# Optimization experiments

Hardware: AMD Instinct MI355X
Metric: run time of the kernel (lower is better)

The kernel has to match this reference:

```python
import jax, jax.numpy as jnp
import numpy as np

N_NODES = 100000
N_EDGES = 1600000
IN_FT = 128
OUT_FT = 128


def setup_inputs() -> dict:
    key = jax.random.key(0)
    k1, k2, k3, k4, k5, k6 = jax.random.split(key, 6)
    stdv = 1.0 / np.sqrt(OUT_FT)
    x = jax.random.normal(k1, (N_NODES, IN_FT), dtype=jnp.float32)
    edge_rows = jax.random.randint(k2, (N_EDGES,), 0, N_NODES, dtype=jnp.int32)
    edge_cols = jax.random.randint(k3, (N_EDGES,), 0, N_NODES, dtype=jnp.int32)
    # normalized adjacency values (positive, like D^-1 A)
    edge_vals = jax.random.uniform(k4, (N_EDGES,), dtype=jnp.float32)
    W = jax.random.uniform(k5, (IN_FT, OUT_FT), dtype=jnp.float32, minval=-stdv, maxval=stdv)
    b = jax.random.uniform(k6, (OUT_FT,), dtype=jnp.float32, minval=-stdv, maxval=stdv)
    return {"x": x, "edge_rows": edge_rows, "edge_cols": edge_cols,
            "edge_vals": edge_vals, "W": W, "b": b}


def reference(x, edge_rows, edge_cols, edge_vals, W, b):
    # dense projection + bias: [N, out_ft]
    h = x @ W + b
    # SpMM: out[r] = sum_e vals[e] * h[cols[e]] for edges with rows[e] == r
    msgs = edge_vals[:, None] * h[edge_cols]          # [E, out_ft]
    out = jax.ops.segment_sum(msgs, edge_rows, num_segments=N_NODES)
    return jax.nn.relu(out)
```

## Files before the change

### kernel.cpp

```cpp
#include <hip/hip_runtime.h>

#define N_NODES 100000
#define N_EDGES 1600000
#define FT 128

#define NBUCK 391
#define EPB 4096
#define NBLKP ((N_EDGES + EPB - 1) / EPB)
#define CAP 1536

#define OFF_H 0
#define OFF_BUCKETED 25600000
#define OFF_BLKHIST 38400000
#define OFF_BTOT 39011524
#define OFF_BBASE 39013088
#define WS_NEEDED 39014656

typedef __attribute__((ext_vector_type(8))) short bf16x8;
typedef __attribute__((ext_vector_type(4))) float f32x4;

static __device__ __forceinline__ ushort f2bf(float f) {
  const unsigned u = __float_as_uint(f);
  return (ushort)((u + 0x7FFF + ((u >> 16) & 1)) >> 16);
}
static __device__ __forceinline__ float bf2f(ushort s) {
  return __uint_as_float((unsigned)s << 16);
}

__global__ __launch_bounds__(256) void gemm_bias_kernel(
    const float* __restrict__ x,
    const float* __restrict__ W,
    const float* __restrict__ b,
    ushort* __restrict__ h) {
  __shared__ __align__(16) ushort whi[16384];
  __shared__ __align__(16) ushort wlo[16384];

  const int tid = threadIdx.x;

  for (int idx = tid; idx < 16384; idx += 256) {
    const int k = idx >> 7;
    const int col = idx & 127;
    const float wv = W[idx];
    const ushort hi = f2bf(wv);
    const ushort lo = f2bf(wv - bf2f(hi));
    const int lane_ = (((k >> 3) & 3) << 4) | (col & 15);
    const int pos = ((((k >> 5) << 3) + (col >> 4)) * 64 + lane_) * 8 + (k & 7);
    whi[pos] = hi;
    wlo[pos] = lo;
  }
  __syncthreads();

  const int w = tid >> 6;
  const int lane = tid & 63;
  const int r0 = blockIdx.x * 256 + w * 64;
  const int arow = lane & 15;
  const int kgrp = (lane >> 4) << 3;

  float bias_v[8];
#pragma unroll
  for (int ct = 0; ct < 8; ++ct) bias_v[ct] = b[ct * 16 + (lane & 15)];

  f32x4 acc[4][8];
#pragma unroll
  for (int rf = 0; rf < 4; ++rf)
#pragma unroll
    for (int ct = 0; ct < 8; ++ct) acc[rf][ct] = (f32x4){0.f, 0.f, 0.f, 0.f};

#pragma unroll
  for (int ks = 0; ks < 4; ++ks) {
    bf16x8 afr[4];
#pragma unroll
    for (int rf = 0; rf < 4; ++rf) {
      int r = r0 + rf * 16 + arow;
      r = (r < N_NODES) ? r : (N_NODES - 1);
      const float* xp = x + (size_t)r * FT + ks * 32 + kgrp;
      const float4 u0 = *(const float4*)xp;
      const float4 u1 = *(const float4*)(xp + 4);
      bf16x8 a;
      a[0] = (short)f2bf(u0.x);
      a[1] = (short)f2bf(u0.y);
      a[2] = (short)f2bf(u0.z);
      a[3] = (short)f2bf(u0.w);
      a[4] = (short)f2bf(u1.x);
      a[5] = (short)f2bf(u1.y);
      a[6] = (short)f2bf(u1.z);
      a[7] = (short)f2bf(u1.w);
      afr[rf] = a;
    }
#pragma unroll
    for (int ct = 0; ct < 8; ++ct) {
      const int fo = ((ks * 8 + ct) * 64 + lane) * 8;
      const bf16x8 bh = *(const bf16x8*)&whi[fo];
      const bf16x8 bl = *(const bf16x8*)&wlo[fo];
#pragma unroll
      for (int rf = 0; rf < 4; ++rf) {
        acc[rf][ct] = __builtin_amdgcn_mfma_f32_16x16x32_bf16(
            afr[rf], bh, acc[rf][ct], 0, 0, 0);
        acc[rf][ct] = __builtin_amdgcn_mfma_f32_16x16x32_bf16(
            afr[rf], bl, acc[rf][ct], 0, 0, 0);
      }
    }
  }

  const int crow0 = (lane >> 4) << 2;
  const int ccol = lane & 15;
#pragma unroll
  for (int rf = 0; rf < 4; ++rf) {
#pragma unroll
    for (int ct = 0; ct < 8; ++ct) {
      const int col = ct * 16 + ccol;
#pragma unroll
      for (int i = 0; i < 4; ++i) {
        const int row = r0 + rf * 16 + crow0 + i;
        if (row < N_NODES)
          h[(size_t)row * FT + col] = f2bf(acc[rf][ct][i] + bias_v[ct]);
      }
    }
  }
}

__global__ __launch_bounds__(256) void partA_kernel(
    const int* __restrict__ erows, int* __restrict__ blkhist) {
  __shared__ int cnt[NBUCK];
  const int tid = threadIdx.x;
  for (int j = tid; j < NBUCK; j += 256) cnt[j] = 0;
  __syncthreads();

  const int base4 = blockIdx.x * (EPB / 4);
#pragma unroll
  for (int it = 0; it < EPB / 4 / 256; ++it) {
    const int idx4 = base4 + it * 256 + tid;
    if (idx4 < N_EDGES / 4) {
      const int4 r = ((const int4*)erows)[idx4];
      atomicAdd(&cnt[r.x >> 8], 1);
      atomicAdd(&cnt[r.y >> 8], 1);
      atomicAdd(&cnt[r.z >> 8], 1);
      atomicAdd(&cnt[r.w >> 8], 1);
    }
  }
  __syncthreads();
  int* dst = blkhist + (size_t)blockIdx.x * NBUCK;
  for (int j = tid; j < NBUCK; j += 256) dst[j] = cnt[j];
}

__global__ __launch_bounds__(512) void partB1_kernel(
    int* __restrict__ blkhist, int* __restrict__ btot) {
  __shared__ int ps[512];
  const int b = blockIdx.x;
  const int t = threadIdx.x;
  int v = 0;
  if (t < NBLKP) v = blkhist[(size_t)t * NBUCK + b];
  ps[t] = v;
  __syncthreads();
#pragma unroll
  for (int d = 1; d < 512; d <<= 1) {
    const int u = (t >= d) ? ps[t - d] : 0;
    __syncthreads();
    ps[t] += u;
    __syncthreads();
  }
  if (t < NBLKP) blkhist[(size_t)t * NBUCK + b] = ps[t] - v;
  if (t == NBLKP - 1) btot[b] = ps[t];
}

__global__ __launch_bounds__(512) void partB2_kernel(
    const int* __restrict__ btot, int* __restrict__ bucket_base) {
  __shared__ int ps[512];
  const int t = threadIdx.x;
  int v = (t < NBUCK) ? btot[t] : 0;
  ps[t] = v;
  __syncthreads();
#pragma unroll
  for (int d = 1; d < 512; d <<= 1) {
    const int u = (t >= d) ? ps[t - d] : 0;
    __syncthreads();
    ps[t] += u;
    __syncthreads();
  }
  if (t < NBUCK) bucket_base[t] = ps[t] - v;
  if (t == NBUCK - 1) bucket_base[NBUCK] = N_EDGES;
}

__global__ __launch_bounds__(256) void partC_kernel(
    const int* __restrict__ erows,
    const int* __restrict__ ecols,
    const float* __restrict__ evals,
    const int* __restrict__ blkhist,
    const int* __restrict__ bucket_base,
    int2* __restrict__ bucketed) {
  __shared__ int cur[NBUCK];
  const int tid = threadIdx.x;
  const int* src = blkhist + (size_t)blockIdx.x * NBUCK;
  for (int j = tid; j < NBUCK; j += 256) cur[j] = src[j] + bucket_base[j];
  __syncthreads();

  const int base4 = blockIdx.x * (EPB / 4);
#pragma unroll
  for (int it = 0; it < EPB / 4 / 256; ++it) {
    const int idx4 = base4 + it * 256 + tid;
    if (idx4 < N_EDGES / 4) {
      const int4 r = ((const int4*)erows)[idx4];
      const int4 c = ((const int4*)ecols)[idx4];
      const float4 v = ((const float4*)evals)[idx4];
      int p;
      p = atomicAdd(&cur[r.x >> 8], 1);
      bucketed[p] = (int2){((r.x & 255) << 24) | c.x, __float_as_int(v.x)};
      p = atomicAdd(&cur[r.y >> 8], 1);
      bucketed[p] = (int2){((r.y & 255) << 24) | c.y, __float_as_int(v.y)};
      p = atomicAdd(&cur[r.z >> 8], 1);
      bucketed[p] = (int2){((r.z & 255) << 24) | c.z, __float_as_int(v.z)};
      p = atomicAdd(&cur[r.w >> 8], 1);
      bucketed[p] = (int2){((r.w & 255) << 24) | c.w, __float_as_int(v.w)};
    }
  }
}

__global__ __launch_bounds__(512) void spmm_bucket_kernel(
    const int2* __restrict__ bucketed,
    const int* __restrict__ bucket_base,
    const ushort* __restrict__ h,
    float* __restrict__ out) {
  __shared__ int2 tmp[CAP];
  __shared__ int2 eds[CAP];
  __shared__ int cnt[64];
  __shared__ int pos[64];
  __shared__ int cur[64];
  __shared__ int ns;
  const int b = blockIdx.x >> 2;
  const int q = blockIdx.x & 3;
  const int t = threadIdx.x;
  const int beg = bucket_base[b];
  const int end = bucket_base[b + 1];

  if (t < 64) cnt[t] = 0;
  if (t == 0) ns = 0;
  __syncthreads();

  for (int i = beg + t; i < end; i += 512) {
    const int2 rec = bucketed[i];
    const int r8 = ((unsigned)rec.x) >> 24;
    if ((r8 >> 6) == q) {
      const int p = atomicAdd(&ns, 1);
      if (p < CAP) {
        tmp[p] = rec;
        atomicAdd(&cnt[r8 & 63], 1);
      }
    }
  }
  __syncthreads();

  const int m = (ns < CAP) ? ns : CAP;
  const bool overflow = (ns > CAP);

  if (t < 64) pos[t] = cnt[t];
  __syncthreads();
#pragma unroll
  for (int d = 1; d < 64; d <<= 1) {
    int u = 0;
    if (t < 64 && t >= d) u = pos[t - d];
    __syncthreads();
    if (t < 64) pos[t] += u;
    __syncthreads();
  }
  if (t < 64) {
    const int excl = pos[t] - cnt[t];
    pos[t] = excl;
    cur[t] = excl;
  }
  __syncthreads();

  for (int i = t; i < m; i += 512) {
    const int2 rec = tmp[i];
    const int r6 = (((unsigned)rec.x) >> 24) & 63;
    const int p = atomicAdd(&cur[r6], 1);
    eds[p] = (int2){rec.x & 0x00FFFFFF, rec.y};
  }
  __syncthreads();

  const int g = t >> 5;
  const int lane = t & 31;
  const int j = lane * 4;

  for (int rr = 0; rr < 4; ++rr) {
    const int r = rr * 16 + g;
    const int row = b * 256 + q * 64 + r;
    const int rbeg = pos[r];
    const int rend = cur[r];

    float a0 = 0.f, a1 = 0.f, a2 = 0.f, a3 = 0.f;
    int e = rbeg;
    for (; e + 3 < rend; e += 4) {
      const int2 p0 = eds[e];
      const int2 p1 = eds[e + 1];
      const int2 p2 = eds[e + 2];
      const int2 p3 = eds[e + 3];
      const ushort4 q0 = *(const ushort4*)(h + (size_t)p0.x * FT + j);
      const ushort4 q1 = *(const ushort4*)(h + (size_t)p1.x * FT + j);
      const ushort4 q2 = *(const ushort4*)(h + (size_t)p2.x * FT + j);
      const ushort4 q3 = *(const ushort4*)(h + (size_t)p3.x * FT + j);
      const float v0 = __int_as_float(p0.y);
      const float v1 = __int_as_float(p1.y);
      const float v2 = __int_as_float(p2.y);
      const float v3 = __int_as_float(p3.y);
      a0 = fmaf(v0, bf2f(q0.x), a0);
      a1 = fmaf(v0, bf2f(q0.y), a1);
      a2 = fmaf(v0, bf2f(q0.z), a2);
      a3 = fmaf(v0, bf2f(q0.w), a3);
      a0 = fmaf(v1, bf2f(q1.x), a0);
      a1 = fmaf(v1, bf2f(q1.y), a1);
      a2 = fmaf(v1, bf2f(q1.z), a2);
      a3 = fmaf(v1, bf2f(q1.w), a3);
      a0 = fmaf(v2, bf2f(q2.x), a0);
      a1 = fmaf(v2, bf2f(q2.y), a1);
      a2 = fmaf(v2, bf2f(q2.z), a2);
      a3 = fmaf(v2, bf2f(q2.w), a3);
      a0 = fmaf(v3, bf2f(q3.x), a0);
      a1 = fmaf(v3, bf2f(q3.y), a1);
      a2 = fmaf(v3, bf2f(q3.z), a2);
      a3 = fmaf(v3, bf2f(q3.w), a3);
    }
    for (; e < rend; ++e) {
      const int2 p0 = eds[e];
      const float v0 = __int_as_float(p0.y);
      const ushort4 q0 = *(const ushort4*)(h + (size_t)p0.x * FT + j);
      a0 = fmaf(v0, bf2f(q0.x), a0);
      a1 = fmaf(v0, bf2f(q0.y), a1);
      a2 = fmaf(v0, bf2f(q0.z), a2);
      a3 = fmaf(v0, bf2f(q0.w), a3);
    }
    if (overflow) {
      int seen = 0;
      const int have = rend - rbeg;
      for (int i = beg; i < end; ++i) {
        const int2 rec = bucketed[i];
        const int r8 = ((unsigned)rec.x) >> 24;
        if ((r8 >> 6) == q && (r8 & 63) == r) {
          ++seen;
          if (seen > have) {
            const float v0 = __int_as_float(rec.y);
            const ushort4 q0 =
                *(const ushort4*)(h + (size_t)(rec.x & 0x00FFFFFF) * FT + j);
            a0 = fmaf(v0, bf2f(q0.x), a0);
            a1 = fmaf(v0, bf2f(q0.y), a1);
            a2 = fmaf(v0, bf2f(q0.z), a2);
            a3 = fmaf(v0, bf2f(q0.w), a3);
          }
        }
      }
    }

    if (row < N_NODES) {
      float4 o;
      o.x = fmaxf(a0, 0.f);
      o.y = fmaxf(a1, 0.f);
      o.z = fmaxf(a2, 0.f);
      o.w = fmaxf(a3, 0.f);
      *(float4*)(out + (size_t)row * FT + j) = o;
    }
  }
}

__global__ __launch_bounds__(256) void edge_scatter_kernel(
    const int* __restrict__ erows,
    const int* __restrict__ ecols,
    const float* __restrict__ evals,
    const ushort* __restrict__ h,
    float* out) {
  const int tid = threadIdx.x;
  const int e = blockIdx.x * 8 + (tid >> 5);
  if (e >= N_EDGES) return;
  const int r = erows[e];
  const int c = ecols[e];
  const float v = evals[e];
  const int j = (tid & 31) * 4;
  const ushort4 q = *(const ushort4*)(h + (size_t)c * FT + j);
  float* op = out + (size_t)r * FT + j;
  atomicAdd(op + 0, v * bf2f(q.x));
  atomicAdd(op + 1, v * bf2f(q.y));
  atomicAdd(op + 2, v * bf2f(q.z));
  atomicAdd(op + 3, v * bf2f(q.w));
}

__global__ __launch_bounds__(256) void relu_kernel(float* out, int n4) {
  const int i = blockIdx.x * blockDim.x + threadIdx.x;
  if (i < n4) {
    float4 v = ((float4*)out)[i];
    v.x = fmaxf(v.x, 0.f);
    v.y = fmaxf(v.y, 0.f);
    v.z = fmaxf(v.z, 0.f);
    v.w = fmaxf(v.w, 0.f);
    ((float4*)out)[i] = v;
  }
}

extern "C" void kernel_launch(void* const* d_in, const int* in_sizes, int n_in,
                              void* d_out, int out_size, void* d_ws, size_t ws_size,
                              hipStream_t stream) {
  const float* x = (const float*)d_in[0];
  const int* erows = (const int*)d_in[1];
  const int* ecols = (const int*)d_in[2];
  const float* evals = (const float*)d_in[3];
  const float* W = (const float*)d_in[4];
  const float* b = (const float*)d_in[5];
  float* out = (float*)d_out;

  char* ws = (char*)d_ws;
  ushort* h = (ushort*)(ws + OFF_H);

  gemm_bias_kernel<<<(N_NODES + 255) / 256, 256, 0, stream>>>(x, W, b, h);

  if (ws_size >= (size_t)WS_NEEDED) {
    int2* bucketed = (int2*)(ws + OFF_BUCKETED);
    int* blkhist = (int*)(ws + OFF_BLKHIST);
    int* btot = (int*)(ws + OFF_BTOT);
    int* bucket_base = (int*)(ws + OFF_BBASE);

    partA_kernel<<<NBLKP, 256, 0, stream>>>(erows, blkhist);
    partB1_kernel<<<NBUCK, 512, 0, stream>>>(blkhist, btot);
    partB2_kernel<<<1, 512, 0, stream>>>(btot, bucket_base);
    partC_kernel<<<NBLKP, 256, 0, stream>>>(erows, ecols, evals, blkhist,
                                            bucket_base, bucketed);
    spmm_bucket_kernel<<<NBUCK * 4, 512, 0, stream>>>(bucketed, bucket_base,
                                                      h, out);
  } else {
    hipMemsetAsync(d_out, 0, (size_t)out_size * sizeof(float), stream);
    edge_scatter_kernel<<<(N_EDGES + 7) / 8, 256, 0, stream>>>(erows, ecols,
                                                               evals, h, out);
    const int n4 = out_size / 4;
    relu_kernel<<<(n4 + 255) / 256, 256, 0, stream>>>(out, n4);
  }
}
```

Baseline: 123.3 us.

## Fuse projection GEMM with edge bucketing kernel and drop bf16 low-part correction

Merges the dense x@W+b projection into the same launch as the partC edge-scatter pass, with the first blocks computing the GEMM and the remaining blocks bucketing edges, so the two independent stages overlap and one launch disappears. The split hi/lo bf16 representation of W is dropped, halving MFMA count and LDS use for the weight tile. This trades accuracy of the projection for speed, and the fused kernel's shared-memory footprint now applies to bucketing blocks as well.

```diff
diff --git a/kernel.cpp b/kernel.cpp
--- a/kernel.cpp
+++ b/kernel.cpp
@@ -8,6 +8,7 @@
 #define EPB 4096
 #define NBLKP ((N_EDGES + EPB - 1) / EPB)
 #define CAP 1536
+#define GEMM_BLOCKS ((N_NODES + 255) / 256)
 
 #define OFF_H 0
 #define OFF_BUCKETED 25600000
@@ -25,98 +26,6 @@
 }
 static __device__ __forceinline__ float bf2f(ushort s) {
   return __uint_as_float((unsigned)s << 16);
-}
-
-__global__ __launch_bounds__(256) void gemm_bias_kernel(
-    const float* __restrict__ x,
-    const float* __restrict__ W,
-    const float* __restrict__ b,
-    ushort* __restrict__ h) {
-  __shared__ __align__(16) ushort whi[16384];
-  __shared__ __align__(16) ushort wlo[16384];
-
-  const int tid = threadIdx.x;
-
-  for (int idx = tid; idx < 16384; idx += 256) {
-    const int k = idx >> 7;
-    const int col = idx & 127;
-    const float wv = W[idx];
-    const ushort hi = f2bf(wv);
-    const ushort lo = f2bf(wv - bf2f(hi));
-    const int lane_ = (((k >> 3) & 3) << 4) | (col & 15);
-    const int pos = ((((k >> 5) << 3) + (col >> 4)) * 64 + lane_) * 8 + (k & 7);
-    whi[pos] = hi;
-    wlo[pos] = lo;
-  }
-  __syncthreads();
-
-  const int w = tid >> 6;
-  const int lane = tid & 63;
-  const int r0 = blockIdx.x * 256 + w * 64;
-  const int arow = lane & 15;
-  const int kgrp = (lane >> 4) << 3;
-
-  float bias_v[8];
-#pragma unroll
-  for (int ct = 0; ct < 8; ++ct) bias_v[ct] = b[ct * 16 + (lane & 15)];
-
-  f32x4 acc[4][8];
-#pragma unroll
-  for (int rf = 0; rf < 4; ++rf)
-#pragma unroll
-    for (int ct = 0; ct < 8; ++ct) acc[rf][ct] = (f32x4){0.f, 0.f, 0.f, 0.f};
-
-#pragma unroll
-  for (int ks = 0; ks < 4; ++ks) {
-    bf16x8 afr[4];
-#pragma unroll
-    for (int rf = 0; rf < 4; ++rf) {
-      int r = r0 + rf * 16 + arow;
-      r = (r < N_NODES) ? r : (N_NODES - 1);
-      const float* xp = x + (size_t)r * FT + ks * 32 + kgrp;
-      const float4 u0 = *(const float4*)xp;
-      const float4 u1 = *(const float4*)(xp + 4);
-      bf16x8 a;
-      a[0] = (short)f2bf(u0.x);
-      a[1] = (short)f2bf(u0.y);
-      a[2] = (short)f2bf(u0.z);
-      a[3] = (short)f2bf(u0.w);
-      a[4] = (short)f2bf(u1.x);
-      a[5] = (short)f2bf(u1.y);
-      a[6] = (short)f2bf(u1.z);
-      a[7] = (short)f2bf(u1.w);
-      afr[rf] = a;
-    }
-#pragma unroll
-    for (int ct = 0; ct < 8; ++ct) {
-      const int fo = ((ks * 8 + ct) * 64 + lane) * 8;
-      const bf16x8 bh = *(const bf16x8*)&whi[fo];
-      const bf16x8 bl = *(const bf16x8*)&wlo[fo];
-#pragma unroll
-      for (int rf = 0; rf < 4; ++rf) {
-        acc[rf][ct] = __builtin_amdgcn_mfma_f32_16x16x32_bf16(
-            afr[rf], bh, acc[rf][ct], 0, 0, 0);
-        acc[rf][ct] = __builtin_amdgcn_mfma_f32_16x16x32_bf16(
-            afr[rf], bl, acc[rf][ct], 0, 0, 0);
-      }
-    }
-  }
-
-  const int crow0 = (lane >> 4) << 2;
-  const int ccol = lane & 15;
-#pragma unroll
-  for (int rf = 0; rf < 4; ++rf) {
-#pragma unroll
-    for (int ct = 0; ct < 8; ++ct) {
-      const int col = ct * 16 + ccol;
-#pragma unroll
-      for (int i = 0; i < 4; ++i) {
-        const int row = r0 + rf * 16 + crow0 + i;
-        if (row < N_NODES)
-          h[(size_t)row * FT + col] = f2bf(acc[rf][ct][i] + bias_v[ct]);
-      }
-    }
-  }
 }
 
 __global__ __launch_bounds__(256) void partA_kernel(
@@ -181,36 +90,121 @@
   if (t == NBUCK - 1) bucket_base[NBUCK] = N_EDGES;
 }
 
-__global__ __launch_bounds__(256) void partC_kernel(
+__global__ __launch_bounds__(256) void fused_gemm_partC_kernel(
+    const float* __restrict__ x,
+    const float* __restrict__ W,
+    const float* __restrict__ b,
+    ushort* __restrict__ h,
     const int* __restrict__ erows,
     const int* __restrict__ ecols,
     const float* __restrict__ evals,
     const int* __restrict__ blkhist,
     const int* __restrict__ bucket_base,
     int2* __restrict__ bucketed) {
+  __shared__ __align__(16) ushort whi[16384];
   __shared__ int cur[NBUCK];
   const int tid = threadIdx.x;
-  const int* src = blkhist + (size_t)blockIdx.x * NBUCK;
-  for (int j = tid; j < NBUCK; j += 256) cur[j] = src[j] + bucket_base[j];
-  __syncthreads();
-
-  const int base4 = blockIdx.x * (EPB / 4);
-#pragma unroll
-  for (int it = 0; it < EPB / 4 / 256; ++it) {
-    const int idx4 = base4 + it * 256 + tid;
-    if (idx4 < N_EDGES / 4) {
-      const int4 r = ((const int4*)erows)[idx4];
-      const int4 c = ((const int4*)ecols)[idx4];
-      const float4 v = ((const float4*)evals)[idx4];
-      int p;
-      p = atomicAdd(&cur[r.x >> 8], 1);
-      bucketed[p] = (int2){((r.x & 255) << 24) | c.x, __float_as_int(v.x)};
-      p = atomicAdd(&cur[r.y >> 8], 1);
-      bucketed[p] = (int2){((r.y & 255) << 24) | c.y, __float_as_int(v.y)};
-      p = atomicAdd(&cur[r.z >> 8], 1);
-      bucketed[p] = (int2){((r.z & 255) << 24) | c.z, __float_as_int(v.z)};
-      p = atomicAdd(&cur[r.w >> 8], 1);
-      bucketed[p] = (int2){((r.w & 255) << 24) | c.w, __float_as_int(v.w)};
+
+  if (blockIdx.x < GEMM_BLOCKS) {
+    for (int idx = tid; idx < 16384; idx += 256) {
+      const int k = idx >> 7;
+      const int col = idx & 127;
+      const ushort hi = f2bf(W[idx]);
+      const int lane_ = (((k >> 3) & 3) << 4) | (col & 15);
+      const int pos =
+          ((((k >> 5) << 3) + (col >> 4)) * 64 + lane_) * 8 + (k & 7);
+      whi[pos] = hi;
+    }
+    __syncthreads();
+
+    const int w = tid >> 6;
+    const int lane = tid & 63;
+    const int r0 = blockIdx.x * 256 + w * 64;
+    const int arow = lane & 15;
+    const int kgrp = (lane >> 4) << 3;
+
+    float bias_v[8];
+#pragma unroll
+    for (int ct = 0; ct < 8; ++ct) bias_v[ct] = b[ct * 16 + (lane & 15)];
+
+    f32x4 acc[4][8];
+#pragma unroll
+    for (int rf = 0; rf < 4; ++rf)
+#pragma unroll
+      for (int ct = 0; ct < 8; ++ct) acc[rf][ct] = (f32x4){0.f, 0.f, 0.f, 0.f};
+
+#pragma unroll
+    for (int ks = 0; ks < 4; ++ks) {
+      bf16x8 afr[4];
+#pragma unroll
+      for (int rf = 0; rf < 4; ++rf) {
+        int r = r0 + rf * 16 + arow;
+        r = (r < N_NODES) ? r : (N_NODES - 1);
+        const float* xp = x + (size_t)r * FT + ks * 32 + kgrp;
+        const float4 u0 = *(const float4*)xp;
+        const float4 u1 = *(const float4*)(xp + 4);
+        bf16x8 a;
+        a[0] = (short)f2bf(u0.x);
+        a[1] = (short)f2bf(u0.y);
+        a[2] = (short)f2bf(u0.z);
+        a[3] = (short)f2bf(u0.w);
+        a[4] = (short)f2bf(u1.x);
+        a[5] = (short)f2bf(u1.y);
+        a[6] = (short)f2bf(u1.z);
+        a[7] = (short)f2bf(u1.w);
+        afr[rf] = a;
+      }
+#pragma unroll
+      for (int ct = 0; ct < 8; ++ct) {
+        const int fo = ((ks * 8 + ct) * 64 + lane) * 8;
+        const bf16x8 bh = *(const bf16x8*)&whi[fo];
+#pragma unroll
+        for (int rf = 0; rf < 4; ++rf) {
+          acc[rf][ct] = __builtin_amdgcn_mfma_f32_16x16x32_bf16(
+              afr[rf], bh, acc[rf][ct], 0, 0, 0);
+        }
+      }
+    }
+
+    const int crow0 = (lane >> 4) << 2;
+    const int ccol = lane & 15;
+#pragma unroll
+    for (int rf = 0; rf < 4; ++rf) {
+#pragma unroll
+      for (int ct = 0; ct < 8; ++ct) {
+        const int col = ct * 16 + ccol;
+#pragma unroll
+        for (int i = 0; i < 4; ++i) {
+          const int row = r0 + rf * 16 + crow0 + i;
+          if (row < N_NODES)
+            h[(size_t)row * FT + col] = f2bf(acc[rf][ct][i] + bias_v[ct]);
+        }
+      }
+    }
+  } else {
+    const int bid = blockIdx.x - GEMM_BLOCKS;
+    const int* src = blkhist + (size_t)bid * NBUCK;
+    for (int j = tid; j < NBUCK; j += 256) cur[j] = src[j] + bucket_base[j];
+    __syncthreads();
+
+    const int base4 = bid * (EPB / 4);
+#pragma unroll
+    for (int it = 0; it < EPB / 4 / 256; ++it) {
+      const int idx4 = base4 + it * 256 + tid;
+      if (idx4 < N_EDGES / 4) {
+        const int4 r = ((const int4*)erows)[idx4];
+        const int4 c = ((const int4*)ecols)[idx4];
+        const float4 v = ((const float4*)evals)[idx4];
+        int p;
+        p = atomicAdd(&cur[r.x >> 8], 1);
+        bucketed[p] = (int2){((r.x & 255) << 24) | c.x, __float_as_int(v.x)};
+        p = atomicAdd(&cur[r.y >> 8], 1);
+        bucketed[p] = (int2){((r.y & 255) << 24) | c.y, __float_as_int(v.y)};
+        p = atomicAdd(&cur[r.z >> 8], 1);
+        bucketed[p] = (int2){((r.z & 255) << 24) | c.z, __float_as_int(v.z)};
+        p = atomicAdd(&cur[r.w >> 8], 1);
+        bucketed[p] = (int2){((r.w & 255) << 24) | c.w, __float_as_int(v.w)};
+      }
     }
   }
 }
@@ -360,6 +354,90 @@
   }
 }
 
+__global__ __launch_bounds__(256) void gemm_bias_kernel(
+    const float* __restrict__ x,
+    const float* __restrict__ W,
+    const float* __restrict__ b,
+    ushort* __restrict__ h) {
+  __shared__ __align__(16) ushort whi[16384];
+  const int tid = threadIdx.x;
+
+  for (int idx = tid; idx < 16384; idx += 256) {
+    const int k = idx >> 7;
+    const int col = idx & 127;
+    const ushort hi = f2bf(W[idx]);
+    const int lane_ = (((k >> 3) & 3) << 4) | (col & 15);
+    const int pos = ((((k >> 5) << 3) + (col >> 4)) * 64 + lane_) * 8 + (k & 7);
+    whi[pos] = hi;
+  }
+  __syncthreads();
+
+  const int w = tid >> 6;
+  const int lane = tid & 63;
+  const int r0 = blockIdx.x * 256 + w * 64;
+  const int arow = lane & 15;
+  const int kgrp = (lane >> 4) << 3;
+
+  float bias_v[8];
+#pragma unroll
+  for (int ct = 0; ct < 8; ++ct) bias_v[ct] = b[ct * 16 + (lane & 15)];
+
+  f32x4 acc[4][8];
+#pragma unroll
+  for (int rf = 0; rf < 4; ++rf)
+#pragma unroll
+    for (int ct = 0; ct < 8; ++ct) acc[rf][ct] = (f32x4){0.f, 0.f, 0.f, 0.f};
+
+#pragma unroll
+  for (int ks = 0; ks < 4; ++ks) {
+    bf16x8 afr[4];
+#pragma unroll
+    for (int rf = 0; rf < 4; ++rf) {
+      int r = r0 + rf * 16 + arow;
+      r = (r < N_NODES) ? r : (N_NODES - 1);
+      const float* xp = x + (size_t)r * FT + ks * 32 + kgrp;
+      const float4 u0 = *(const float4*)xp;
+      const float4 u1 = *(const float4*)(xp + 4);
+      bf16x8 a;
+      a[0] = (short)f2bf(u0.x);
+      a[1] = (short)f2bf(u0.y);
+      a[2] = (short)f2bf(u0.z);
+      a[3] = (short)f2bf(u0.w);
+      a[4] = (short)f2bf(u1.x);
+      a[5] = (short)f2bf(u1.y);
+      a[6] = (short)f2bf(u1.z);
+      a[7] = (short)f2bf(u1.w);
+      afr[rf] = a;
+    }
+#pragma unroll
+    for (int ct = 0; ct < 8; ++ct) {
+      const int fo = ((ks * 8 + ct) * 64 + lane) * 8;
+      const bf16x8 bh = *(const bf16x8*)&whi[fo];
+#pragma unroll
+      for (int rf = 0; rf < 4; ++rf) {
+        acc[rf][ct] = __builtin_amdgcn_mfma_f32_16x16x32_bf16(
+            afr[rf], bh, acc[rf][ct], 0, 0, 0);
+      }
+    }
+  }
+
+  const int crow0 = (lane >> 4) << 2;
+  const int ccol = lane & 15;
+#pragma unroll
+  for (int rf = 0; rf < 4; ++rf) {
+#pragma unroll
+    for (int ct = 0; ct < 8; ++ct) {
+      const int col = ct * 16 + ccol;
+#pragma unroll
+      for (int i = 0; i < 4; ++i) {
+        const int row = r0 + rf * 16 + crow0 + i;
+        if (row < N_NODES)
+          h[(size_t)row * FT + col] = f2bf(acc[rf][ct][i] + bias_v[ct]);
+      }
+    }
+  }
+}
+
 __global__ __launch_bounds__(256) void edge_scatter_kernel(
     const int* __restrict__ erows,
     const int* __restrict__ ecols,
@@ -407,8 +485,6 @@
   char* ws = (char*)d_ws;
   ushort* h = (ushort*)(ws + OFF_H);
 
-  gemm_bias_kernel<<<(N_NODES + 255) / 256, 256, 0, stream>>>(x, W, b, h);
-
   if (ws_size >= (size_t)WS_NEEDED) {
     int2* bucketed = (int2*)(ws + OFF_BUCKETED);
     int* blkhist = (int*)(ws + OFF_BLKHIST);
@@ -418,11 +494,12 @@
     partA_kernel<<<NBLKP, 256, 0, stream>>>(erows, blkhist);
     partB1_kernel<<<NBUCK, 512, 0, stream>>>(blkhist, btot);
     partB2_kernel<<<1, 512, 0, stream>>>(btot, bucket_base);
-    partC_kernel<<<NBLKP, 256, 0, stream>>>(erows, ecols, evals, blkhist,
-                                            bucket_base, bucketed);
+    fused_gemm_partC_kernel<<<GEMM_BLOCKS + NBLKP, 256, 0, stream>>>(
+        x, W, b, h, erows, ecols, evals, blkhist, bucket_base, bucketed);
     spmm_bucket_kernel<<<NBUCK * 4, 512, 0, stream>>>(bucketed, bucket_base,
                                                       h, out);
   } else {
+    gemm_bias_kernel<<<GEMM_BLOCKS, 256, 0, stream>>>(x, W, b, h);
     hipMemsetAsync(d_out, 0, (size_t)out_size * sizeof(float), stream);
     edge_scatter_kernel<<<(N_EDGES + 7) / 8, 256, 0, stream>>>(erows, ecols,
                                                                evals, h, out);
```

After: 117.8 us. 4.5% less time.
